# Kernel optimization log

Measured on AMD Instinct MI355X. Metric: run time of the kernel, lower is better.

Reference implementation:

```python
import jax, jax.numpy as jnp
import numpy as np

B, C, W, H = 8192, 512, 14, 4
D = C // H  # head dim = 128


def setup_inputs() -> dict:
    key = jax.random.key(0)
    ks = jax.random.split(key, 8)
    s = 1.0 / np.sqrt(C).astype(np.float32)
    return {
        "x": jax.random.normal(ks[0], (B, C, W), jnp.float32),
        "Wq": jax.random.normal(ks[1], (C, C), jnp.float32) * s,
        "bq": jax.random.normal(ks[2], (C,), jnp.float32) * 0.01,
        "Wk": jax.random.normal(ks[3], (C, C), jnp.float32) * s,
        "bk": jax.random.normal(ks[4], (C,), jnp.float32) * 0.01,
        "Wv": jax.random.normal(ks[5], (C, C), jnp.float32) * s,
        "bv": jax.random.normal(ks[6], (C,), jnp.float32) * 0.01,
        "rel_w": jax.random.normal(ks[7], (1, H, D, W), jnp.float32),
    }


def reference(x, Wq, bq, Wk, bk, Wv, bv, rel_w):
    # Conv1d(kernel_size=1) == channel-wise linear: out[b,o,w] = sum_c Wm[o,c]*x[b,c,w] + bm[o]
    def proj(Wm, bm):
        y = jnp.einsum('oc,bcw->bow', Wm, x) + bm[None, :, None]
        return y.reshape(B, H, D, W)

    q = proj(Wq, bq)  # [B,H,D,W]
    k = proj(Wk, bk)
    v = proj(Wv, bv)

    # content-content: q^T k over head dim -> [B,H,W,W]
    cc = jnp.einsum('bhdi,bhdj->bhij', q, k)
    # content-position: rel_w^T q -> [B,H,W,W] (rows = relative position, cols = query pos)
    cp = jnp.einsum('hdi,bhdj->bhij', rel_w[0], q)

    attn = jax.nn.softmax(cc + cp, axis=-1)  # softmax over last dim, as in the original

    # out = v @ attn^T : out[b,h,d,i] = sum_j v[b,h,d,j] * attn[b,h,i,j]
    out = jnp.einsum('bhdj,bhij->bhdi', v, attn)
    return out.reshape(B, C, W)
```

## Files before the change

### kernel.cpp

```cpp
#include <hip/hip_runtime.h>
#include <hip/hip_bf16.h>

typedef __bf16 bf16x8 __attribute__((ext_vector_type(8)));
typedef float f32x4 __attribute__((ext_vector_type(4)));
typedef int i32x4 __attribute__((ext_vector_type(4)));

typedef __attribute__((address_space(1))) const void GVoid;
typedef __attribute__((address_space(3))) void LVoid;

#define SX1 16.0f
#define SX1I 0.0625f
#define SX2 4000.0f
#define SW1 400.0f
#define SW1I 0.0025f
#define SW2 100000.0f
#define SR1 32.0f
#define SR1I 0.03125f
#define SR2 8000.0f
#define SC_QK 1.5625e-4f
#define SC_CP 1.953125e-3f
#define CORR 0.004f

static __device__ __forceinline__ float b2f(unsigned short u) {
    union { float f; unsigned int i; } x; x.i = ((unsigned int)u) << 16; return x.f;
}
static __device__ __forceinline__ unsigned short f2b(float f) {
    union { float f; unsigned int u; } x; x.f = f;
    unsigned int r = x.u + 0x7FFFu + ((x.u >> 16) & 1u);
    return (unsigned short)(r >> 16);
}
static __device__ __forceinline__ int q8v(float v, float s) {
    int i = __float2int_rn(v * s);
    return (i > 127) ? 127 : (i < -127 ? -127 : i);
}

__global__ __launch_bounds__(256) void k_prep(const float* __restrict__ Wq, const float* __restrict__ Wk,
                                              const float* __restrict__ Wv, const float* __restrict__ bq,
                                              const float* __restrict__ bk, const float* __restrict__ bv,
                                              const float* __restrict__ relw, char* __restrict__ Wi8,
                                              float* __restrict__ biasA) {
    int o = blockIdx.x;
    int tid = threadIdx.x;
    if (o < 1024) {
        const float* src = (o < 512) ? (Wq + (long)o * 512) : (Wk + (long)(o - 512) * 512);
        char* row = Wi8 + (long)o * 1024;
        for (int c = tid; c < 512; c += 256) {
            float w = src[c];
            int wh = q8v(w, SW1);
            float res = w - (float)wh * SW1I;
            int wl = q8v(res, SW2);
            row[c] = (char)wh;
            row[512 + c] = (char)wl;
        }
    } else if (o < 1536) {
        const float* src = Wv + (long)(o - 1024) * 512;
        char* row = Wi8 + (long)(1152 + (o - 1024)) * 1024;
        for (int c = tid; c < 512; c += 256) {
            float w = src[c];
            int wh = q8v(w, SW1);
            float res = w - (float)wh * SW1I;
            int wl = q8v(res, SW2);
            row[c] = (char)wh;
            row[512 + c] = (char)wl;
        }
    } else if (o < 1592) {
        int t = o - 1536, h = t / 14, i = t - h * 14;
        char* row = Wi8 + (long)(1024 + t) * 1024;
#pragma unroll
        for (int cc = 0; cc < 2; ++cc) {
            int c = tid + cc * 256;
            float acc = 0.f;
            for (int d = 0; d < 128; ++d)
                acc += relw[h * 1792 + d * 14 + i] * Wq[(long)(h * 128 + d) * 512 + c];
            int rh = q8v(acc, SR1);
            float res = acc - (float)rh * SR1I;
            int rl = q8v(res, SR2);
            row[c] = (char)rh;
            row[512 + c] = (char)rl;
        }
        if (tid == 0) {
            float acc = 0.f;
            for (int d = 0; d < 128; ++d) acc += relw[h * 1792 + d * 14 + i] * bq[h * 128 + d];
            biasA[1024 + t] = acc;
        }
    } else {
        for (int i = tid; i < 1664; i += 256) {
            if (i >= 1024 && i < 1080) continue;
            biasA[i] = (i < 512) ? bq[i] : (i < 1024) ? bk[i - 512] : (i < 1152) ? 0.f : bv[i - 1152];
        }
        int* z = (int*)(Wi8 + (long)1080 * 1024);
        for (int idx = tid; idx < 72 * 256; idx += 256) z[idx] = 0;
    }
}

__global__ __launch_bounds__(256) void k_transpose(const float* __restrict__ x,
                                                   char* __restrict__ Ai8, int b0) {
    __shared__ float xl[512 * 15];
    const float* xb = x + (long)(b0 + blockIdx.x) * 7168;
    const float4* xb4 = (const float4*)xb;
    int tid = threadIdx.x;
#pragma unroll
    for (int it = 0; it < 7; ++it) {
        int f = tid + it * 256;
        float4 v = xb4[f];
        float vals[4] = {v.x, v.y, v.z, v.w};
        int e = f * 4;
#pragma unroll
        for (int j = 0; j < 4; ++j) {
            int ee = e + j;
            int c = (ee * 9363) >> 17;
            int w = ee - c * 14;
            xl[c * 15 + w] = vals[j];
        }
    }
    __syncthreads();
    char* irow = Ai8 + (long)blockIdx.x * 14336;
#pragma unroll
    for (int it = 0; it < 7; ++it) {
        int p = tid + it * 256;
        int w = p >> 7, c0 = (p & 127) * 4;
        unsigned int hp = 0, lp = 0;
#pragma unroll
        for (int j = 0; j < 4; ++j) {
            float v = xl[(c0 + j) * 15 + w];
            int xh = q8v(v, SX1);
            float res = v - (float)xh * SX1I;
            int xlo = q8v(res, SX2);
            hp |= ((unsigned int)(xh & 255)) << (8 * j);
            lp |= ((unsigned int)(xlo & 255)) << (8 * j);
        }
        *(unsigned int*)(irow + (long)w * 1024 + c0) = hp;
        *(unsigned int*)(irow + (long)w * 1024 + 512 + c0) = lp;
    }
}

__global__ __launch_bounds__(256, 2) void k_gemmA(const char* __restrict__ Ai8,
                                                  const char* __restrict__ Wi8,
                                                  const float* __restrict__ biasA,
                                                  float* __restrict__ qkf,
                                                  unsigned short* __restrict__ vb, int Mtiles) {
    __shared__ __align__(16) char Ahs[128 * 128];
    __shared__ __align__(16) char Als[128 * 128];
    __shared__ __align__(16) char Bhs[128 * 128];
    __shared__ __align__(16) char Bls[128 * 128];
    int nwg = Mtiles * 13;
    int p = blockIdx.x;
    int xcd = p & 7, o8 = p >> 3;
    int q8_ = nwg >> 3, r8 = nwg & 7;
    int t = (xcd < r8 ? xcd * (q8_ + 1) : r8 * (q8_ + 1) + (xcd - r8) * q8_) + o8;
    int mt = t / 13, nt = t - mt * 13;
    long m0 = (long)mt * 128;
    int n0 = nt * 128;
    int tid = threadIdx.x, lane = tid & 63, wv = tid >> 6;
    int wr = wv >> 1, wc = wv & 1;
    int rrow = lane >> 3;
    int u = lane & 7;

    i32x4 accM[4][4], accC[4][4];
#pragma unroll
    for (int i = 0; i < 4; ++i)
#pragma unroll
        for (int j = 0; j < 4; ++j) { accM[i][j] = (i32x4){0, 0, 0, 0}; accC[i][j] = (i32x4){0, 0, 0, 0}; }

    for (int kt = 0; kt < 4; ++kt) {
        int kof = kt * 128;
#pragma unroll
        for (int ti = 0; ti < 4; ++ti) {
            int chunk = wv * 4 + ti;
            int row = chunk * 8 + rrow;
            int gu = ((u ^ (row & 7)) << 4);
            const char* sa = Ai8 + ((m0 + row) << 10) + kof + gu;
            const char* sb = Wi8 + ((long)(n0 + row) << 10) + kof + gu;
            __builtin_amdgcn_global_load_lds((GVoid*)sa, (LVoid*)(Ahs + chunk * 1024), 16, 0, 0);
            __builtin_amdgcn_global_load_lds((GVoid*)(sa + 512), (LVoid*)(Als + chunk * 1024), 16, 0, 0);
            __builtin_amdgcn_global_load_lds((GVoid*)sb, (LVoid*)(Bhs + chunk * 1024), 16, 0, 0);
            __builtin_amdgcn_global_load_lds((GVoid*)(sb + 512), (LVoid*)(Bls + chunk * 1024), 16, 0, 0);
        }
        asm volatile("s_waitcnt vmcnt(0)" ::: "memory");
        __syncthreads();
#pragma unroll
        for (int kk = 0; kk < 2; ++kk) {
            i32x4 ah[4], al[4], bh[4], bl[4];
            int kb = kk * 64 + ((lane >> 4) << 4);
#pragma unroll
            for (int mf = 0; mf < 4; ++mf) {
                int row = wr * 64 + mf * 16 + (lane & 15);
                int off = row * 128 + (kb ^ ((row & 7) << 4));
                ah[mf] = *(const i32x4*)(Ahs + off);
                al[mf] = *(const i32x4*)(Als + off);
            }
#pragma unroll
            for (int nf = 0; nf < 4; ++nf) {
                int row = wc * 64 + nf * 16 + (lane & 15);
                int off = row * 128 + (kb ^ ((row & 7) << 4));
                bh[nf] = *(const i32x4*)(Bhs + off);
                bl[nf] = *(const i32x4*)(Bls + off);
            }
#pragma unroll
            for (int mf = 0; mf < 4; ++mf)
#pragma unroll
                for (int nf = 0; nf < 4; ++nf) {
                    accM[mf][nf] = __builtin_amdgcn_mfma_i32_16x16x64_i8(ah[mf], bh[nf], accM[mf][nf], 0, 0, 0);
                    accC[mf][nf] = __builtin_amdgcn_mfma_i32_16x16x64_i8(ah[mf], bl[nf], accC[mf][nf], 0, 0, 0);
                    accC[mf][nf] = __builtin_amdgcn_mfma_i32_16x16x64_i8(al[mf], bh[nf], accC[mf][nf], 0, 0, 0);
                }
        }
        __syncthreads();
    }
#pragma unroll
    for (int nf = 0; nf < 4; ++nf) {
        int n = n0 + wc * 64 + nf * 16 + (lane & 15);
        float scale = (n < 1024) ? SC_QK : (n < 1152 ? SC_CP : SC_QK);
        float bb = biasA[n];
#pragma unroll
        for (int mf = 0; mf < 4; ++mf) {
            long mg = m0 + wr * 64 + mf * 16 + ((lane >> 4) << 2);
#pragma unroll
            for (int r = 0; r < 4; ++r) {
                float val = ((float)accM[mf][nf][r] + CORR * (float)accC[mf][nf][r]) * scale + bb;
                if (n < 1080) qkf[(mg + r) * 1152 + n] = val;
                else if (n >= 1152) vb[(mg + r) * 512 + (n - 1152)] = f2b(val);
            }
        }
    }
}

__global__ __launch_bounds__(512) void k_attn(const float* __restrict__ qkf,
                                              const unsigned short* __restrict__ vb,
                                              float* __restrict__ out, int b0) {
    __shared__ float qs[14 * 512];
    __shared__ float ks[14 * 512];
    __shared__ float cps[56 * 16];
    __shared__ float sl[56 * 16];
    __shared__ unsigned short vs[14 * 512];
    int tid = threadIdx.x;
    long mb = (long)blockIdx.x * 14;
    const float4* qk4 = (const float4*)qkf;
#pragma unroll
    for (int it = 0; it < 7; ++it) {
        int idx = tid + it * 512;
        int w = idx >> 8, c4 = idx & 255;
        float4 v = qk4[(mb + w) * 288 + c4];
        if (c4 < 128) *(float4*)&qs[w * 512 + ((c4 ^ (w & 7)) << 2)] = v;
        else {
            int uu = c4 - 128;
            *(float4*)&ks[w * 512 + ((uu ^ (w & 7)) << 2)] = v;
        }
    }
#pragma unroll
    for (int it = 0; it < 2; ++it) {
        int idx = tid + it * 512;
        if (idx < 784) {
            int w = idx / 56, tt = idx - w * 56;
            cps[tt * 16 + w] = qkf[(mb + w) * 1152 + 1024 + tt];
        }
    }
#pragma unroll
    for (int it = 0; it < 2; ++it) {
        int idx = tid + it * 512;
        if (idx < 896) {
            int w = idx >> 6, uu = idx & 63;
            *(uint4*)&vs[w * 512 + uu * 8] = *(const uint4*)&vb[(mb + w) * 512 + uu * 8];
        }
    }
    __syncthreads();
    if (tid < 196) {
        int h = tid / 49, r = tid - h * 49;
        int i0 = (r / 7) * 2, j0 = (r - (r / 7) * 7) * 2;
        float a00 = 0.f, a01 = 0.f, a10 = 0.f, a11 = 0.f;
#pragma unroll
        for (int d4 = 0; d4 < 32; ++d4) {
            int uu = h * 32 + d4;
            float4 qa = *(const float4*)&qs[i0 * 512 + ((uu ^ (i0 & 7)) << 2)];
            float4 qb = *(const float4*)&qs[(i0 + 1) * 512 + ((uu ^ ((i0 + 1) & 7)) << 2)];
            float4 ka = *(const float4*)&ks[j0 * 512 + ((uu ^ (j0 & 7)) << 2)];
            float4 kb = *(const float4*)&ks[(j0 + 1) * 512 + ((uu ^ ((j0 + 1) & 7)) << 2)];
            a00 += qa.x * ka.x + qa.y * ka.y + qa.z * ka.z + qa.w * ka.w;
            a01 += qa.x * kb.x + qa.y * kb.y + qa.z * kb.z + qa.w * kb.w;
            a10 += qb.x * ka.x + qb.y * ka.y + qb.z * ka.z + qb.w * ka.w;
            a11 += qb.x * kb.x + qb.y * kb.y + qb.z * kb.z + qb.w * kb.w;
        }
        int base = (h * 14 + i0) * 16 + j0;
        sl[base] = a00 + cps[base];
        sl[base + 1] = a01 + cps[base + 1];
        sl[base + 16] = a10 + cps[base + 16];
        sl[base + 17] = a11 + cps[base + 17];
    }
    __syncthreads();
    if (tid < 56) {
        float* row = &sl[tid * 16];
        float m = row[0];
#pragma unroll
        for (int j = 1; j < 14; ++j) m = fmaxf(m, row[j]);
        float ex[14]; float sum = 0.f;
#pragma unroll
        for (int j = 0; j < 14; ++j) { ex[j] = __expf(row[j] - m); sum += ex[j]; }
        float inv = 1.f / sum;
#pragma unroll
        for (int j = 0; j < 14; ++j) row[j] = ex[j] * inv;
    }
    __syncthreads();
    int c = tid, h = c >> 7;
    float vr[14];
#pragma unroll
    for (int j = 0; j < 14; ++j) vr[j] = b2f(vs[j * 512 + c]);
    float* orow = out + (((long)(b0 + blockIdx.x) * 512 + c) * 14);
    float ob[14];
#pragma unroll
    for (int i = 0; i < 14; ++i) {
        const float* ar = &sl[(h * 14 + i) * 16];
        float a = 0.f;
#pragma unroll
        for (int j = 0; j < 14; ++j) a += vr[j] * ar[j];
        ob[i] = a;
    }
#pragma unroll
    for (int t2 = 0; t2 < 7; ++t2)
        *(float2*)(orow + t2 * 2) = make_float2(ob[2 * t2], ob[2 * t2 + 1]);
}

extern "C" void kernel_launch(void* const* d_in, const int* in_sizes, int n_in,
                              void* d_out, int out_size, void* d_ws, size_t ws_size,
                              hipStream_t stream) {
    const float* x    = (const float*)d_in[0];
    const float* Wq   = (const float*)d_in[1];
    const float* bq   = (const float*)d_in[2];
    const float* Wk   = (const float*)d_in[3];
    const float* bk   = (const float*)d_in[4];
    const float* Wv   = (const float*)d_in[5];
    const float* bv   = (const float*)d_in[6];
    const float* relw = (const float*)d_in[7];
    float* out = (float*)d_out;
    char* ws = (char*)d_ws;

    char*  Wi8   = ws;
    float* biasA = (float*)(ws + 1703936);
    const long WS_DATA = 1712128;

    long avail = (long)ws_size - WS_DATA;
    long nbmax = avail / 93184;
    long NBc = (nbmax / 128) * 128;
    if (NBc > 8192) NBc = 8192;
    if (NBc < 128) NBc = 128;

    char*           Ai8 = ws + WS_DATA;
    float*          qkf = (float*)(Ai8 + NBc * 14336);
    unsigned short* vbw = (unsigned short*)(qkf + NBc * 16128);

    k_prep<<<1593, 256, 0, stream>>>(Wq, Wk, Wv, bq, bk, bv, relw, Wi8, biasA);

    for (int b0 = 0; b0 < 8192; b0 += (int)NBc) {
        int nb = 8192 - b0; if (nb > NBc) nb = (int)NBc;
        int Mtiles = (nb * 14) / 128;
        k_transpose<<<nb, 256, 0, stream>>>(x, Ai8, b0);
        k_gemmA<<<Mtiles * 13, 256, 0, stream>>>(Ai8, Wi8, biasA, qkf, vbw, Mtiles);
        k_attn<<<nb, 512, 0, stream>>>(qkf, vbw, out, b0);
    }
}
```

Before: 731.7 us.

## Double-buffer LDS in int8 projection GEMM with 512-thread workgroups

The GEMM kernel now keeps two LDS buffers and issues the global-to-LDS loads for the next K slice before computing the current one. It waits with a partial vmcnt so those loads overlap the MFMA work. The workgroup grows to 8 waves, each owning a 32x64 output sub-tile instead of 64x64, which lowers per-wave accumulator registers. LDS use doubles to 128KB per block, so likely only one block fits per CU, and the overlap previously coming from two resident blocks may be lost.

```diff
diff --git a/kernel.cpp b/kernel.cpp
--- a/kernel.cpp
+++ b/kernel.cpp
@@ -134,15 +134,12 @@
     }
 }
 
-__global__ __launch_bounds__(256, 2) void k_gemmA(const char* __restrict__ Ai8,
+__global__ __launch_bounds__(512, 2) void k_gemmA(const char* __restrict__ Ai8,
                                                   const char* __restrict__ Wi8,
                                                   const float* __restrict__ biasA,
                                                   float* __restrict__ qkf,
                                                   unsigned short* __restrict__ vb, int Mtiles) {
-    __shared__ __align__(16) char Ahs[128 * 128];
-    __shared__ __align__(16) char Als[128 * 128];
-    __shared__ __align__(16) char Bhs[128 * 128];
-    __shared__ __align__(16) char Bls[128 * 128];
+    __shared__ __align__(16) char Ls[2][4][128 * 128];
     int nwg = Mtiles * 13;
     int p = blockIdx.x;
     int xcd = p & 7, o8 = p >> 3;
@@ -152,52 +149,66 @@
     long m0 = (long)mt * 128;
     int n0 = nt * 128;
     int tid = threadIdx.x, lane = tid & 63, wv = tid >> 6;
-    int wr = wv >> 1, wc = wv & 1;
-    int rrow = lane >> 3;
-    int u = lane & 7;
-
-    i32x4 accM[4][4], accC[4][4];
-#pragma unroll
-    for (int i = 0; i < 4; ++i)
+    int wm = wv >> 1, wn = wv & 1;
+
+    i32x4 accM[2][4], accC[2][4];
+#pragma unroll
+    for (int i = 0; i < 2; ++i)
 #pragma unroll
         for (int j = 0; j < 4; ++j) { accM[i][j] = (i32x4){0, 0, 0, 0}; accC[i][j] = (i32x4){0, 0, 0, 0}; }
 
+#define STAGE(KT, BUF)                                                                           \
+    {                                                                                            \
+        int kof = (KT) * 128;                                                                    \
+        _Pragma("unroll") for (int i = 0; i < 2; ++i) {                                          \
+            int row = i * 64 + (tid >> 3);                                                       \
+            int gu = (((tid & 7) ^ (row & 7)) << 4);                                             \
+            long ao = ((m0 + row) << 10) + kof + gu;                                             \
+            long bo = ((long)(n0 + row) << 10) + kof + gu;                                       \
+            int dof = i * 8192 + tid * 16;                                                       \
+            __builtin_amdgcn_global_load_lds((GVoid*)(Ai8 + ao), (LVoid*)(&Ls[BUF][0][0] + dof), 16, 0, 0); \
+            __builtin_amdgcn_global_load_lds((GVoid*)(Ai8 + ao + 512), (LVoid*)(&Ls[BUF][1][0] + dof), 16, 0, 0); \
+            __builtin_amdgcn_global_load_lds((GVoid*)(Wi8 + bo), (LVoid*)(&Ls[BUF][2][0] + dof), 16, 0, 0); \
+            __builtin_amdgcn_global_load_lds((GVoid*)(Wi8 + bo + 512), (LVoid*)(&Ls[BUF][3][0] + dof), 16, 0, 0); \
+        }                                                                                        \
+    }
+
+    STAGE(0, 0);
+    int cur = 0;
     for (int kt = 0; kt < 4; ++kt) {
-        int kof = kt * 128;
-#pragma unroll
-        for (int ti = 0; ti < 4; ++ti) {
-            int chunk = wv * 4 + ti;
-            int row = chunk * 8 + rrow;
-            int gu = ((u ^ (row & 7)) << 4);
-            const char* sa = Ai8 + ((m0 + row) << 10) + kof + gu;
-            const char* sb = Wi8 + ((long)(n0 + row) << 10) + kof + gu;
-            __builtin_amdgcn_global_load_lds((GVoid*)sa, (LVoid*)(Ahs + chunk * 1024), 16, 0, 0);
-            __builtin_amdgcn_global_load_lds((GVoid*)(sa + 512), (LVoid*)(Als + chunk * 1024), 16, 0, 0);
-            __builtin_amdgcn_global_load_lds((GVoid*)sb, (LVoid*)(Bhs + chunk * 1024), 16, 0, 0);
-            __builtin_amdgcn_global_load_lds((GVoid*)(sb + 512), (LVoid*)(Bls + chunk * 1024), 16, 0, 0);
-        }
-        asm volatile("s_waitcnt vmcnt(0)" ::: "memory");
-        __syncthreads();
+        if (kt < 3) {
+            if (cur == 0) STAGE(kt + 1, 1) else STAGE(kt + 1, 0);
+            asm volatile("s_waitcnt vmcnt(8)" ::: "memory");
+        } else {
+            asm volatile("s_waitcnt vmcnt(0)" ::: "memory");
+        }
+        __builtin_amdgcn_s_barrier();
+        __builtin_amdgcn_sched_barrier(0);
+
+        const char* Ah = &Ls[cur][0][0];
+        const char* Al = &Ls[cur][1][0];
+        const char* Bh = &Ls[cur][2][0];
+        const char* Bl = &Ls[cur][3][0];
 #pragma unroll
         for (int kk = 0; kk < 2; ++kk) {
-            i32x4 ah[4], al[4], bh[4], bl[4];
+            i32x4 ah[2], al[2], bh[4], bl[4];
             int kb = kk * 64 + ((lane >> 4) << 4);
 #pragma unroll
-            for (int mf = 0; mf < 4; ++mf) {
-                int row = wr * 64 + mf * 16 + (lane & 15);
+            for (int mf = 0; mf < 2; ++mf) {
+                int row = wm * 32 + mf * 16 + (lane & 15);
                 int off = row * 128 + (kb ^ ((row & 7) << 4));
-                ah[mf] = *(const i32x4*)(Ahs + off);
-                al[mf] = *(const i32x4*)(Als + off);
+                ah[mf] = *(const i32x4*)(Ah + off);
+                al[mf] = *(const i32x4*)(Al + off);
             }
 #pragma unroll
             for (int nf = 0; nf < 4; ++nf) {
-                int row = wc * 64 + nf * 16 + (lane & 15);
+                int row = wn * 64 + nf * 16 + (lane & 15);
                 int off = row * 128 + (kb ^ ((row & 7) << 4));
-                bh[nf] = *(const i32x4*)(Bhs + off);
-                bl[nf] = *(const i32x4*)(Bls + off);
+                bh[nf] = *(const i32x4*)(Bh + off);
+                bl[nf] = *(const i32x4*)(Bl + off);
             }
 #pragma unroll
-            for (int mf = 0; mf < 4; ++mf)
+            for (int mf = 0; mf < 2; ++mf)
 #pragma unroll
                 for (int nf = 0; nf < 4; ++nf) {
                     accM[mf][nf] = __builtin_amdgcn_mfma_i32_16x16x64_i8(ah[mf], bh[nf], accM[mf][nf], 0, 0, 0);
@@ -205,16 +216,20 @@
                     accC[mf][nf] = __builtin_amdgcn_mfma_i32_16x16x64_i8(al[mf], bh[nf], accC[mf][nf], 0, 0, 0);
                 }
         }
-        __syncthreads();
-    }
+        __builtin_amdgcn_sched_barrier(0);
+        __builtin_amdgcn_s_barrier();
+        cur ^= 1;
+    }
+#undef STAGE
+
 #pragma unroll
     for (int nf = 0; nf < 4; ++nf) {
-        int n = n0 + wc * 64 + nf * 16 + (lane & 15);
+        int n = n0 + wn * 64 + nf * 16 + (lane & 15);
         float scale = (n < 1024) ? SC_QK : (n < 1152 ? SC_CP : SC_QK);
         float bb = biasA[n];
 #pragma unroll
-        for (int mf = 0; mf < 4; ++mf) {
-            long mg = m0 + wr * 64 + mf * 16 + ((lane >> 4) << 2);
+        for (int mf = 0; mf < 2; ++mf) {
+            long mg = m0 + wm * 32 + mf * 16 + ((lane >> 4) << 2);
 #pragma unroll
             for (int r = 0; r < 4; ++r) {
                 float val = ((float)accM[mf][nf][r] + CORR * (float)accC[mf][nf][r]) * scale + bb;
@@ -353,7 +368,7 @@
         int nb = 8192 - b0; if (nb > NBc) nb = (int)NBc;
         int Mtiles = (nb * 14) / 128;
         k_transpose<<<nb, 256, 0, stream>>>(x, Ai8, b0);
-        k_gemmA<<<Mtiles * 13, 256, 0, stream>>>(Ai8, Wi8, biasA, qkf, vbw, Mtiles);
+        k_gemmA<<<Mtiles * 13, 512, 0, stream>>>(Ai8, Wi8, biasA, qkf, vbw, Mtiles);
         k_attn<<<nb, 512, 0, stream>>>(qkf, vbw, out, b0);
     }
 }
```

New measurement: 728.7 us. About the same (-0.4%).
